# Kernel tuning notes

Measured on AMD Instinct MI355X. Metric: run time of the kernel, lower is better.

Reference implementation:

```python
import jax, jax.numpy as jnp
import numpy as np

N_NODES = 2048


def setup_inputs() -> dict:
    key = jax.random.key(0)
    ks = jax.random.split(key, 10)
    s = 0.05
    return {
        "x": jax.random.normal(ks[0], (N_NODES, 32), dtype=jnp.float32),
        "centroids": jax.random.normal(ks[1], (N_NODES, 3), dtype=jnp.float32),
        "W_self1": jax.random.normal(ks[2], (35, 64), dtype=jnp.float32) * s,
        "W_neigh1": jax.random.normal(ks[3], (35, 64), dtype=jnp.float32) * s,
        "b1": jnp.zeros((64,), dtype=jnp.float32),
        "W_self2": jax.random.normal(ks[4], (64, 32), dtype=jnp.float32) * s,
        "W_neigh2": jax.random.normal(ks[5], (64, 32), dtype=jnp.float32) * s,
        "b2": jnp.zeros((32,), dtype=jnp.float32),
        "Wm1": jax.random.normal(ks[6], (64, 32), dtype=jnp.float32) * s,
        "bm1": jnp.zeros((32,), dtype=jnp.float32),
        "Wm2": jax.random.normal(ks[7], (32, 2), dtype=jnp.float32) * s,
        "bm2": jnp.zeros((2,), dtype=jnp.float32),
    }


def reference(x, centroids, W_self1, W_neigh1, b1, W_self2, W_neigh2, b2,
              Wm1, bm1, Wm2, bm2):
    n = x.shape[0]
    # Complete DAG edge list: edges i -> j for all i < j (static indices).
    src, dst = jnp.triu_indices(n, k=1)  # each [E], E = n(n-1)/2

    # --- edge features: per-feature cosine-sim vector + |centroid diff| ---
    norms = jnp.linalg.norm(x, axis=1)                       # [N]
    cos = (x[src] * x[dst]) / (norms[src] * norms[dst])[:, None]   # [E,32]
    cdiff = jnp.abs(centroids[src] - centroids[dst])               # [E,3]
    edge_weight = jnp.concatenate([cos, cdiff], axis=1)            # [E,35]

    h = jnp.concatenate([x, centroids], axis=1)                    # [N,35]

    # in-degree of each destination node (mean aggregator denominator)
    deg = jnp.zeros((n,), dtype=h.dtype).at[dst].add(1.0)
    inv_deg = jnp.where(deg > 0, 1.0 / jnp.maximum(deg, 1.0), 0.0)[:, None]

    # --- SAGEConv 1 (mean, with per-feature edge weights) ---
    msg1 = h[src] * edge_weight                                    # [E,35]
    neigh1 = jax.ops.segment_sum(msg1, dst, num_segments=n) * inv_deg
    h1 = h @ W_self1 + neigh1 @ W_neigh1 + b1                      # [N,64]

    # --- SAGEConv 2 (mean, no edge weight) ---
    neigh2 = jax.ops.segment_sum(h1[src], dst, num_segments=n) * inv_deg
    h2 = h1 @ W_self2 + neigh2 @ W_neigh2 + b2                     # [N,32]

    # --- pairwise edge gather + MLP head ---
    ef = jnp.concatenate([h2[src], h2[dst]], axis=1)               # [E,64]
    hid = jax.nn.relu(ef @ Wm1 + bm1)                              # [E,32]
    out = jax.nn.softmax(hid @ Wm2 + bm2, axis=-1)                 # [E,2]
    return out
```

## Files before the change

### kernel.cpp

```cpp
#include <hip/hip_runtime.h>
#include <math.h>

#define N_NODES 2048
#define N1S 36

__device__ __forceinline__ float invdeg(int j) { return j > 0 ? 1.0f / (float)j : 0.0f; }

__global__ __launch_bounds__(256) void k_edgefeat(const float* __restrict__ x,
                                                  const float* __restrict__ cent,
                                                  float* __restrict__ n1) {
  const int tid = threadIdx.x;
  const int bx = blockIdx.x;
  if (bx < 32) {
    __shared__ float invn_s[N_NODES];
    __shared__ float sc[256];
    const int f = bx;
    for (int r = 0; r < 8; ++r) {
      int n = tid + 256 * r;
      const float4* xp = (const float4*)(x + n * 32);
      float s = 0.f;
#pragma unroll
      for (int q = 0; q < 8; ++q) {
        float4 v = xp[q];
        s += v.x * v.x + v.y * v.y + v.z * v.z + v.w * v.w;
      }
      invn_s[n] = rsqrtf(s);
    }
    __syncthreads();
    float sv[8], xv[8];
    float ts = 0.f;
#pragma unroll
    for (int r = 0; r < 8; ++r) {
      int i = tid * 8 + r;
      float xf = x[i * 32 + f];
      xv[r] = xf;
      float s = xf * xf * invn_s[i];
      sv[r] = s;
      ts += s;
    }
    sc[tid] = ts;
    __syncthreads();
    for (int off = 1; off < 256; off <<= 1) {
      float v = (tid >= off) ? sc[tid - off] : 0.f;
      __syncthreads();
      sc[tid] += v;
      __syncthreads();
    }
    float P = sc[tid] - ts;
#pragma unroll
    for (int r = 0; r < 8; ++r) {
      int i = tid * 8 + r;
      n1[i * N1S + f] = P * xv[r] * invn_s[i] * invdeg(i);
      P += sv[r];
    }
  } else {
    __shared__ float cs[N_NODES * 3];
    const float4* cp = (const float4*)cent;
    float4* csp = (float4*)cs;
#pragma unroll
    for (int q = 0; q < 6; ++q) csp[tid + 256 * q] = cp[tid + 256 * q];
    __syncthreads();
    const int w = (bx - 32) * 4 + (tid >> 6);
    const int lane = tid & 63;
#pragma unroll
    for (int pick = 0; pick < 2; ++pick) {
      const int j = pick ? (2047 - w) : w;
      const float cj0 = cs[j * 3 + 0], cj1 = cs[j * 3 + 1], cj2 = cs[j * 3 + 2];
      float s0 = 0.f, s1 = 0.f, s2 = 0.f;
      for (int i = lane; i < j; i += 64) {
        float c0 = cs[i * 3 + 0], c1 = cs[i * 3 + 1], c2 = cs[i * 3 + 2];
        s0 += c0 * fabsf(c0 - cj0);
        s1 += c1 * fabsf(c1 - cj1);
        s2 += c2 * fabsf(c2 - cj2);
      }
#pragma unroll
      for (int d = 32; d > 0; d >>= 1) {
        s0 += __shfl_down(s0, d);
        s1 += __shfl_down(s1, d);
        s2 += __shfl_down(s2, d);
      }
      if (lane == 0) {
        float idg = invdeg(j);
        n1[j * N1S + 32] = s0 * idg;
        n1[j * N1S + 33] = s1 * idg;
        n1[j * N1S + 34] = s2 * idg;
      }
    }
  }
}

__global__ __launch_bounds__(256) void k_h1(const float* __restrict__ x,
                                            const float* __restrict__ cent,
                                            const float* __restrict__ n1,
                                            const float* __restrict__ Ws1,
                                            const float* __restrict__ Wn1,
                                            const float* __restrict__ b1,
                                            float* __restrict__ h1,
                                            float* __restrict__ h1T) {
  const int tid = threadIdx.x;
  const int n = __builtin_amdgcn_readfirstlane(blockIdx.x * 4 + (tid >> 6));
  const int o = tid & 63;
  float acc = b1[o];
  const float4* xr = (const float4*)(x + n * 32);
  const float4* nr = (const float4*)(n1 + n * N1S);
#pragma unroll
  for (int q = 0; q < 8; ++q) {
    float4 xv = xr[q];
    float4 nv = nr[q];
    acc += xv.x * Ws1[(4 * q + 0) * 64 + o] + nv.x * Wn1[(4 * q + 0) * 64 + o];
    acc += xv.y * Ws1[(4 * q + 1) * 64 + o] + nv.y * Wn1[(4 * q + 1) * 64 + o];
    acc += xv.z * Ws1[(4 * q + 2) * 64 + o] + nv.z * Wn1[(4 * q + 2) * 64 + o];
    acc += xv.w * Ws1[(4 * q + 3) * 64 + o] + nv.w * Wn1[(4 * q + 3) * 64 + o];
  }
  {
    float4 nv = nr[8];
    float c0 = cent[n * 3 + 0], c1 = cent[n * 3 + 1], c2 = cent[n * 3 + 2];
    acc += c0 * Ws1[32 * 64 + o] + nv.x * Wn1[32 * 64 + o];
    acc += c1 * Ws1[33 * 64 + o] + nv.y * Wn1[33 * 64 + o];
    acc += c2 * Ws1[34 * 64 + o] + nv.z * Wn1[34 * 64 + o];
  }
  h1[n * 64 + o] = acc;
  h1T[o * N_NODES + n] = acc;
}

__global__ __launch_bounds__(256) void k_scan_h1(const float* __restrict__ h1T,
                                                 float* __restrict__ n2) {
  __shared__ float sc[256];
  const int tid = threadIdx.x;
  const int o = blockIdx.x;
  float sv[8];
  const float4* colp = (const float4*)(h1T + o * N_NODES);
  float4 a = colp[2 * tid];
  float4 b = colp[2 * tid + 1];
  sv[0] = a.x; sv[1] = a.y; sv[2] = a.z; sv[3] = a.w;
  sv[4] = b.x; sv[5] = b.y; sv[6] = b.z; sv[7] = b.w;
  float ts = 0.f;
#pragma unroll
  for (int r = 0; r < 8; ++r) ts += sv[r];
  sc[tid] = ts;
  __syncthreads();
  for (int off = 1; off < 256; off <<= 1) {
    float v = (tid >= off) ? sc[tid - off] : 0.f;
    __syncthreads();
    sc[tid] += v;
    __syncthreads();
  }
  float P = sc[tid] - ts;
#pragma unroll
  for (int r = 0; r < 8; ++r) {
    int i = tid * 8 + r;
    n2[i * 64 + o] = P * invdeg(i);
    P += sv[r];
  }
}

__global__ __launch_bounds__(256) void k_h2AB(const float* __restrict__ h1,
                                              const float* __restrict__ n2,
                                              const float* __restrict__ Ws2,
                                              const float* __restrict__ Wn2,
                                              const float* __restrict__ b2,
                                              const float* __restrict__ Wm1,
                                              const float* __restrict__ bm1,
                                              float* __restrict__ A,
                                              float* __restrict__ Bm) {
  __shared__ float h2s[4][32];
  const int tid = threadIdx.x;
  const int wv = tid >> 6;
  const int lane = tid & 63;
  const int o = lane & 31;
  const int half = lane >> 5;
  const int n = __builtin_amdgcn_readfirstlane(blockIdx.x * 4 + wv);
  float acc = b2[o];
#pragma unroll
  for (int f = 0; f < 64; ++f)
    acc += h1[n * 64 + f] * Ws2[f * 32 + o] + n2[n * 64 + f] * Wn2[f * 32 + o];
  h2s[wv][o] = acc;
  __syncthreads();
  float r = half ? bm1[o] : 0.f;
#pragma unroll
  for (int f = 0; f < 32; ++f)
    r += h2s[wv][f] * Wm1[(half * 32 + f) * 32 + o];
  if (half)
    Bm[n * 32 + o] = r;
  else
    A[n * 32 + o] = r;
}

__global__ __launch_bounds__(256) void k_edges(const float* __restrict__ A,
                                               const float* __restrict__ Bm,
                                               const float* __restrict__ Wm2,
                                               const float* __restrict__ bm2,
                                               float2* __restrict__ out) {
  const int tid = threadIdx.x;
  const int j0 = blockIdx.x * 256;
  const int i0 = blockIdx.y * 8;
  if (i0 >= j0 + 255) return;
  const int j = j0 + tid;
  float Br[32];
  const float4* bp = (const float4*)(Bm + j * 32);
#pragma unroll
  for (int q = 0; q < 8; ++q) {
    float4 v = bp[q];
    Br[4 * q + 0] = v.x;
    Br[4 * q + 1] = v.y;
    Br[4 * q + 2] = v.z;
    Br[4 * q + 3] = v.w;
  }
  float wd[32];
#pragma unroll
  for (int f = 0; f < 32; ++f)
    wd[f] = Wm2[f * 2 + 1] - Wm2[f * 2];
  const float db = bm2[1] - bm2[0];
#pragma unroll
  for (int ii = 0; ii < 8; ++ii) {
    const int i = i0 + ii;
    const float* Ar = A + i * 32;
    float d = db;
#pragma unroll
    for (int f = 0; f < 32; ++f)
      d += fmaxf(Ar[f] + Br[f], 0.f) * wd[f];
    if (i < j) {
      float p0 = 1.0f / (1.0f + __expf(d));
      int e = i * (2 * N_NODES - 1 - i) / 2 + (j - i - 1);
      out[e] = make_float2(p0, 1.0f - p0);
    }
  }
}

extern "C" void kernel_launch(void* const* d_in, const int* in_sizes, int n_in,
                              void* d_out, int out_size, void* d_ws, size_t ws_size,
                              hipStream_t stream) {
  const float* x    = (const float*)d_in[0];
  const float* cent = (const float*)d_in[1];
  const float* Ws1  = (const float*)d_in[2];
  const float* Wn1  = (const float*)d_in[3];
  const float* b1   = (const float*)d_in[4];
  const float* Ws2  = (const float*)d_in[5];
  const float* Wn2  = (const float*)d_in[6];
  const float* b2   = (const float*)d_in[7];
  const float* Wm1  = (const float*)d_in[8];
  const float* bm1  = (const float*)d_in[9];
  const float* Wm2  = (const float*)d_in[10];
  const float* bm2  = (const float*)d_in[11];

  float* ws  = (float*)d_ws;
  float* n1  = ws;
  float* h1  = n1 + 2048 * N1S;
  float* h1T = h1 + 2048 * 64;
  float* n2  = h1T + 2048 * 64;
  float* A   = n2 + 2048 * 64;
  float* Bm  = A + 2048 * 32;

  k_edgefeat<<<288, 256, 0, stream>>>(x, cent, n1);
  k_h1<<<512, 256, 0, stream>>>(x, cent, n1, Ws1, Wn1, b1, h1, h1T);
  k_scan_h1<<<64, 256, 0, stream>>>(h1T, n2);
  k_h2AB<<<512, 256, 0, stream>>>(h1, n2, Ws2, Wn2, b2, Wm1, bm1, A, Bm);
  k_edges<<<dim3(8, 256), 256, 0, stream>>>(A, Bm, Wm2, bm2, (float2*)d_out);
}
```

Baseline: 119.9 us.

## Fuse all five stages into one persistent kernel with global barriers

Merges the five separate kernel launches into a single persistent kernel of 256 blocks, using atomic-counter grid barriers between stages and a memset to reset the counters. Work in each stage is redistributed over the fixed grid, and the triangular edge tiles are enumerated linearly. The aim is to remove launch overhead and inter-kernel gaps. In exchange it adds spin-wait barrier cost and lowers per-stage parallelism, and the barrier assumes all 256 blocks are co-resident.

```diff
diff --git a/kernel.cpp b/kernel.cpp
--- a/kernel.cpp
+++ b/kernel.cpp
@@ -3,17 +3,39 @@
 
 #define N_NODES 2048
 #define N1S 36
+#define NB  256
 
 __device__ __forceinline__ float invdeg(int j) { return j > 0 ? 1.0f / (float)j : 0.0f; }
 
-__global__ __launch_bounds__(256) void k_edgefeat(const float* __restrict__ x,
-                                                  const float* __restrict__ cent,
-                                                  float* __restrict__ n1) {
+__device__ __forceinline__ void gbar(int* bar, int idx) {
+  __syncthreads();
+  if (threadIdx.x == 0) {
+    __hip_atomic_fetch_add(&bar[idx], 1, __ATOMIC_ACQ_REL, __HIP_MEMORY_SCOPE_AGENT);
+    while (__hip_atomic_load(&bar[idx], __ATOMIC_ACQUIRE, __HIP_MEMORY_SCOPE_AGENT) < NB)
+      __builtin_amdgcn_s_sleep(1);
+  }
+  __syncthreads();
+}
+
+__global__ __launch_bounds__(256) void k_fused(
+    const float* __restrict__ x, const float* __restrict__ cent,
+    const float* __restrict__ Ws1, const float* __restrict__ Wn1,
+    const float* __restrict__ b1, const float* __restrict__ Ws2,
+    const float* __restrict__ Wn2, const float* __restrict__ b2,
+    const float* __restrict__ Wm1, const float* __restrict__ bm1,
+    const float* __restrict__ Wm2, const float* __restrict__ bm2,
+    float* __restrict__ n1, float* __restrict__ h1, float* __restrict__ h1T,
+    float* __restrict__ n2, float* __restrict__ A, float* __restrict__ Bm,
+    int* bar, float2* __restrict__ out) {
+  __shared__ float smem[6144];
   const int tid = threadIdx.x;
   const int bx = blockIdx.x;
+  const int wv = tid >> 6;
+  const int lane = tid & 63;
+
   if (bx < 32) {
-    __shared__ float invn_s[N_NODES];
-    __shared__ float sc[256];
+    float* invn_s = smem;
+    float* sc = smem + 2048;
     const int f = bx;
     for (int r = 0; r < 8; ++r) {
       int n = tid + 256 * r;
@@ -54,175 +76,171 @@
       P += sv[r];
     }
   } else {
-    __shared__ float cs[N_NODES * 3];
+    float* cs = smem;
     const float4* cp = (const float4*)cent;
     float4* csp = (float4*)cs;
 #pragma unroll
     for (int q = 0; q < 6; ++q) csp[tid + 256 * q] = cp[tid + 256 * q];
     __syncthreads();
-    const int w = (bx - 32) * 4 + (tid >> 6);
-    const int lane = tid & 63;
-#pragma unroll
-    for (int pick = 0; pick < 2; ++pick) {
-      const int j = pick ? (2047 - w) : w;
-      const float cj0 = cs[j * 3 + 0], cj1 = cs[j * 3 + 1], cj2 = cs[j * 3 + 2];
-      float s0 = 0.f, s1 = 0.f, s2 = 0.f;
-      for (int i = lane; i < j; i += 64) {
-        float c0 = cs[i * 3 + 0], c1 = cs[i * 3 + 1], c2 = cs[i * 3 + 2];
-        s0 += c0 * fabsf(c0 - cj0);
-        s1 += c1 * fabsf(c1 - cj1);
-        s2 += c2 * fabsf(c2 - cj2);
-      }
-#pragma unroll
-      for (int d = 32; d > 0; d >>= 1) {
-        s0 += __shfl_down(s0, d);
-        s1 += __shfl_down(s1, d);
-        s2 += __shfl_down(s2, d);
-      }
-      if (lane == 0) {
-        float idg = invdeg(j);
-        n1[j * N1S + 32] = s0 * idg;
-        n1[j * N1S + 33] = s1 * idg;
-        n1[j * N1S + 34] = s2 * idg;
-      }
-    }
-  }
-}
-
-__global__ __launch_bounds__(256) void k_h1(const float* __restrict__ x,
-                                            const float* __restrict__ cent,
-                                            const float* __restrict__ n1,
-                                            const float* __restrict__ Ws1,
-                                            const float* __restrict__ Wn1,
-                                            const float* __restrict__ b1,
-                                            float* __restrict__ h1,
-                                            float* __restrict__ h1T) {
-  const int tid = threadIdx.x;
-  const int n = __builtin_amdgcn_readfirstlane(blockIdx.x * 4 + (tid >> 6));
-  const int o = tid & 63;
-  float acc = b1[o];
-  const float4* xr = (const float4*)(x + n * 32);
-  const float4* nr = (const float4*)(n1 + n * N1S);
-#pragma unroll
-  for (int q = 0; q < 8; ++q) {
-    float4 xv = xr[q];
-    float4 nv = nr[q];
-    acc += xv.x * Ws1[(4 * q + 0) * 64 + o] + nv.x * Wn1[(4 * q + 0) * 64 + o];
-    acc += xv.y * Ws1[(4 * q + 1) * 64 + o] + nv.y * Wn1[(4 * q + 1) * 64 + o];
-    acc += xv.z * Ws1[(4 * q + 2) * 64 + o] + nv.z * Wn1[(4 * q + 2) * 64 + o];
-    acc += xv.w * Ws1[(4 * q + 3) * 64 + o] + nv.w * Wn1[(4 * q + 3) * 64 + o];
-  }
+    const int wvg = (bx - 32) * 4 + wv;
+#pragma unroll
+    for (int rep = 0; rep < 2; ++rep) {
+      const int p = wvg + rep * 896;
+      if (p < 1024) {
+#pragma unroll
+        for (int pick = 0; pick < 2; ++pick) {
+          const int j = pick ? (2047 - p) : p;
+          const float cj0 = cs[j * 3 + 0], cj1 = cs[j * 3 + 1], cj2 = cs[j * 3 + 2];
+          float s0 = 0.f, s1 = 0.f, s2 = 0.f;
+          for (int i = lane; i < j; i += 64) {
+            float c0 = cs[i * 3 + 0], c1 = cs[i * 3 + 1], c2 = cs[i * 3 + 2];
+            s0 += c0 * fabsf(c0 - cj0);
+            s1 += c1 * fabsf(c1 - cj1);
+            s2 += c2 * fabsf(c2 - cj2);
+          }
+#pragma unroll
+          for (int d = 32; d > 0; d >>= 1) {
+            s0 += __shfl_down(s0, d);
+            s1 += __shfl_down(s1, d);
+            s2 += __shfl_down(s2, d);
+          }
+          if (lane == 0) {
+            float idg = invdeg(j);
+            n1[j * N1S + 32] = s0 * idg;
+            n1[j * N1S + 33] = s1 * idg;
+            n1[j * N1S + 34] = s2 * idg;
+          }
+        }
+      }
+    }
+  }
+  gbar(bar, 0);
+
   {
-    float4 nv = nr[8];
-    float c0 = cent[n * 3 + 0], c1 = cent[n * 3 + 1], c2 = cent[n * 3 + 2];
-    acc += c0 * Ws1[32 * 64 + o] + nv.x * Wn1[32 * 64 + o];
-    acc += c1 * Ws1[33 * 64 + o] + nv.y * Wn1[33 * 64 + o];
-    acc += c2 * Ws1[34 * 64 + o] + nv.z * Wn1[34 * 64 + o];
-  }
-  h1[n * 64 + o] = acc;
-  h1T[o * N_NODES + n] = acc;
-}
-
-__global__ __launch_bounds__(256) void k_scan_h1(const float* __restrict__ h1T,
-                                                 float* __restrict__ n2) {
-  __shared__ float sc[256];
-  const int tid = threadIdx.x;
-  const int o = blockIdx.x;
-  float sv[8];
-  const float4* colp = (const float4*)(h1T + o * N_NODES);
-  float4 a = colp[2 * tid];
-  float4 b = colp[2 * tid + 1];
-  sv[0] = a.x; sv[1] = a.y; sv[2] = a.z; sv[3] = a.w;
-  sv[4] = b.x; sv[5] = b.y; sv[6] = b.z; sv[7] = b.w;
-  float ts = 0.f;
-#pragma unroll
-  for (int r = 0; r < 8; ++r) ts += sv[r];
-  sc[tid] = ts;
-  __syncthreads();
-  for (int off = 1; off < 256; off <<= 1) {
-    float v = (tid >= off) ? sc[tid - off] : 0.f;
-    __syncthreads();
-    sc[tid] += v;
-    __syncthreads();
-  }
-  float P = sc[tid] - ts;
-#pragma unroll
-  for (int r = 0; r < 8; ++r) {
-    int i = tid * 8 + r;
-    n2[i * 64 + o] = P * invdeg(i);
-    P += sv[r];
-  }
-}
-
-__global__ __launch_bounds__(256) void k_h2AB(const float* __restrict__ h1,
-                                              const float* __restrict__ n2,
-                                              const float* __restrict__ Ws2,
-                                              const float* __restrict__ Wn2,
-                                              const float* __restrict__ b2,
-                                              const float* __restrict__ Wm1,
-                                              const float* __restrict__ bm1,
-                                              float* __restrict__ A,
-                                              float* __restrict__ Bm) {
-  __shared__ float h2s[4][32];
-  const int tid = threadIdx.x;
-  const int wv = tid >> 6;
-  const int lane = tid & 63;
-  const int o = lane & 31;
-  const int half = lane >> 5;
-  const int n = __builtin_amdgcn_readfirstlane(blockIdx.x * 4 + wv);
-  float acc = b2[o];
-#pragma unroll
-  for (int f = 0; f < 64; ++f)
-    acc += h1[n * 64 + f] * Ws2[f * 32 + o] + n2[n * 64 + f] * Wn2[f * 32 + o];
-  h2s[wv][o] = acc;
-  __syncthreads();
-  float r = half ? bm1[o] : 0.f;
-#pragma unroll
-  for (int f = 0; f < 32; ++f)
-    r += h2s[wv][f] * Wm1[(half * 32 + f) * 32 + o];
-  if (half)
-    Bm[n * 32 + o] = r;
-  else
-    A[n * 32 + o] = r;
-}
-
-__global__ __launch_bounds__(256) void k_edges(const float* __restrict__ A,
-                                               const float* __restrict__ Bm,
-                                               const float* __restrict__ Wm2,
-                                               const float* __restrict__ bm2,
-                                               float2* __restrict__ out) {
-  const int tid = threadIdx.x;
-  const int j0 = blockIdx.x * 256;
-  const int i0 = blockIdx.y * 8;
-  if (i0 >= j0 + 255) return;
-  const int j = j0 + tid;
-  float Br[32];
-  const float4* bp = (const float4*)(Bm + j * 32);
-#pragma unroll
-  for (int q = 0; q < 8; ++q) {
-    float4 v = bp[q];
-    Br[4 * q + 0] = v.x;
-    Br[4 * q + 1] = v.y;
-    Br[4 * q + 2] = v.z;
-    Br[4 * q + 3] = v.w;
-  }
-  float wd[32];
-#pragma unroll
-  for (int f = 0; f < 32; ++f)
-    wd[f] = Wm2[f * 2 + 1] - Wm2[f * 2];
-  const float db = bm2[1] - bm2[0];
-#pragma unroll
-  for (int ii = 0; ii < 8; ++ii) {
-    const int i = i0 + ii;
-    const float* Ar = A + i * 32;
-    float d = db;
-#pragma unroll
-    for (int f = 0; f < 32; ++f)
-      d += fmaxf(Ar[f] + Br[f], 0.f) * wd[f];
-    if (i < j) {
-      float p0 = 1.0f / (1.0f + __expf(d));
-      int e = i * (2 * N_NODES - 1 - i) / 2 + (j - i - 1);
-      out[e] = make_float2(p0, 1.0f - p0);
+    const int gw = bx * 4 + wv;
+    const int o = lane;
+#pragma unroll
+    for (int r = 0; r < 2; ++r) {
+      const int n = __builtin_amdgcn_readfirstlane(gw + 1024 * r);
+      float acc = b1[o];
+      const float4* xr = (const float4*)(x + n * 32);
+      const float4* nr = (const float4*)(n1 + n * N1S);
+#pragma unroll
+      for (int q = 0; q < 8; ++q) {
+        float4 xv = xr[q];
+        float4 nv = nr[q];
+        acc += xv.x * Ws1[(4 * q + 0) * 64 + o] + nv.x * Wn1[(4 * q + 0) * 64 + o];
+        acc += xv.y * Ws1[(4 * q + 1) * 64 + o] + nv.y * Wn1[(4 * q + 1) * 64 + o];
+        acc += xv.z * Ws1[(4 * q + 2) * 64 + o] + nv.z * Wn1[(4 * q + 2) * 64 + o];
+        acc += xv.w * Ws1[(4 * q + 3) * 64 + o] + nv.w * Wn1[(4 * q + 3) * 64 + o];
+      }
+      {
+        float4 nv = nr[8];
+        float c0 = cent[n * 3 + 0], c1 = cent[n * 3 + 1], c2 = cent[n * 3 + 2];
+        acc += c0 * Ws1[32 * 64 + o] + nv.x * Wn1[32 * 64 + o];
+        acc += c1 * Ws1[33 * 64 + o] + nv.y * Wn1[33 * 64 + o];
+        acc += c2 * Ws1[34 * 64 + o] + nv.z * Wn1[34 * 64 + o];
+      }
+      h1[n * 64 + o] = acc;
+      h1T[o * N_NODES + n] = acc;
+    }
+  }
+  gbar(bar, 1);
+
+  if (bx < 64) {
+    float* sc = smem;
+    const int o = bx;
+    float sv[8];
+    const float4* colp = (const float4*)(h1T + o * N_NODES);
+    float4 a = colp[2 * tid];
+    float4 b = colp[2 * tid + 1];
+    sv[0] = a.x; sv[1] = a.y; sv[2] = a.z; sv[3] = a.w;
+    sv[4] = b.x; sv[5] = b.y; sv[6] = b.z; sv[7] = b.w;
+    float ts = 0.f;
+#pragma unroll
+    for (int r = 0; r < 8; ++r) ts += sv[r];
+    sc[tid] = ts;
+    __syncthreads();
+    for (int off = 1; off < 256; off <<= 1) {
+      float v = (tid >= off) ? sc[tid - off] : 0.f;
+      __syncthreads();
+      sc[tid] += v;
+      __syncthreads();
+    }
+    float P = sc[tid] - ts;
+#pragma unroll
+    for (int r = 0; r < 8; ++r) {
+      int i = tid * 8 + r;
+      n2[i * 64 + o] = P * invdeg(i);
+      P += sv[r];
+    }
+  }
+  gbar(bar, 2);
+
+  {
+    const int gw = bx * 4 + wv;
+    const int o = lane & 31;
+    const int half = lane >> 5;
+#pragma unroll
+    for (int r = 0; r < 2; ++r) {
+      const int n = __builtin_amdgcn_readfirstlane(gw + 1024 * r);
+      float acc = b2[o];
+#pragma unroll
+      for (int f = 0; f < 64; ++f)
+        acc += h1[n * 64 + f] * Ws2[f * 32 + o] + n2[n * 64 + f] * Wn2[f * 32 + o];
+      __syncthreads();
+      smem[wv * 32 + o] = acc;
+      __syncthreads();
+      float rr = half ? bm1[o] : 0.f;
+#pragma unroll
+      for (int f = 0; f < 32; ++f)
+        rr += smem[wv * 32 + f] * Wm1[(half * 32 + f) * 32 + o];
+      if (half)
+        Bm[n * 32 + o] = rr;
+      else
+        A[n * 32 + o] = rr;
+    }
+  }
+  gbar(bar, 3);
+
+  {
+    float wd[32];
+#pragma unroll
+    for (int f = 0; f < 32; ++f) wd[f] = Wm2[f * 2 + 1] - Wm2[f * 2];
+    const float db = bm2[1] - bm2[0];
+    for (int c = bx; c < 1152; c += NB) {
+      int jt = 0;
+#pragma unroll
+      for (int t = 1; t < 8; ++t)
+        if (c >= 16 * t * (t + 1)) jt = t;
+      const int ic = c - 16 * jt * (jt + 1);
+      const int j0 = jt * 256;
+      const int i0 = ic * 8;
+      const int j = j0 + tid;
+      float Br[32];
+      const float4* bp = (const float4*)(Bm + j * 32);
+#pragma unroll
+      for (int q = 0; q < 8; ++q) {
+        float4 v = bp[q];
+        Br[4 * q + 0] = v.x;
+        Br[4 * q + 1] = v.y;
+        Br[4 * q + 2] = v.z;
+        Br[4 * q + 3] = v.w;
+      }
+#pragma unroll
+      for (int ii = 0; ii < 8; ++ii) {
+        const int i = i0 + ii;
+        const float* Ar = A + i * 32;
+        float d = db;
+#pragma unroll
+        for (int f = 0; f < 32; ++f)
+          d += fmaxf(Ar[f] + Br[f], 0.f) * wd[f];
+        if (i < j) {
+          float p0 = 1.0f / (1.0f + __expf(d));
+          int e = i * (2 * N_NODES - 1 - i) / 2 + (j - i - 1);
+          out[e] = make_float2(p0, 1.0f - p0);
+        }
+      }
     }
   }
 }
@@ -243,17 +261,17 @@
   const float* Wm2  = (const float*)d_in[10];
   const float* bm2  = (const float*)d_in[11];
 
-  float* ws  = (float*)d_ws;
-  float* n1  = ws;
+  int* bar = (int*)d_ws;
+  float* base = (float*)((char*)d_ws + 256);
+  float* n1  = base;
   float* h1  = n1 + 2048 * N1S;
   float* h1T = h1 + 2048 * 64;
   float* n2  = h1T + 2048 * 64;
   float* A   = n2 + 2048 * 64;
   float* Bm  = A + 2048 * 32;
 
-  k_edgefeat<<<288, 256, 0, stream>>>(x, cent, n1);
-  k_h1<<<512, 256, 0, stream>>>(x, cent, n1, Ws1, Wn1, b1, h1, h1T);
-  k_scan_h1<<<64, 256, 0, stream>>>(h1T, n2);
-  k_h2AB<<<512, 256, 0, stream>>>(h1, n2, Ws2, Wn2, b2, Wm1, bm1, A, Bm);
-  k_edges<<<dim3(8, 256), 256, 0, stream>>>(A, Bm, Wm2, bm2, (float2*)d_out);
+  hipMemsetAsync(bar, 0, 256, stream);
+  k_fused<<<NB, 256, 0, stream>>>(x, cent, Ws1, Wn1, b1, Ws2, Wn2, b2,
+                                  Wm1, bm1, Wm2, bm2,
+                                  n1, h1, h1T, n2, A, Bm, bar, (float2*)d_out);
 }
```

After: 245.0 us. 2.04x slower.
